# Optimization experiments

Measured on AMD Instinct MI355X. Metric: run time of the kernel, lower is better.

## Reference

```python
import jax, jax.numpy as jnp
import numpy as np

B, C, D, H, W = 2, 128, 16, 16, 16

def setup_inputs() -> dict:
    key = jax.random.key(0)
    ks = jax.random.split(key, 7)
    s = 0.02
    return {
        "x": jax.random.normal(ks[0], (B, C, D, H, W), jnp.float32),
        "Wq": jax.random.normal(ks[1], (C, C), jnp.float32) * s,
        "bq": jax.random.normal(ks[2], (C,), jnp.float32) * s,
        "Wk": jax.random.normal(ks[3], (C, C), jnp.float32) * s,
        "bk": jax.random.normal(ks[4], (C,), jnp.float32) * s,
        "Wv": jax.random.normal(ks[5], (C, C), jnp.float32) * s,
        "bv": jax.random.normal(ks[6], (C,), jnp.float32) * s,
    }

def reference(x, Wq, bq, Wk, bk, Wv, bv):
    b, c, d, h, w = x.shape
    n = d * h * w
    xf = x.reshape(b, c, n)  # [B, C, N]
    # 1x1x1 Conv3d == per-voxel linear over channels
    q = jnp.einsum('oc,bcn->bon', Wq, xf) + bq[None, :, None]
    k = jnp.einsum('oc,bcn->bon', Wk, xf) + bk[None, :, None]
    v = jnp.einsum('oc,bcn->bon', Wv, xf) + bv[None, :, None]
    # energy[b,n,m] = sum_c q[b,c,n] * k[b,c,m]  (no scale, as in source)
    energy = jnp.einsum('bcn,bcm->bnm', q, k)
    attention = jax.nn.softmax(energy, axis=-1)
    # out[b,c,n] = sum_m v[b,c,m] * attention[b,n,m]
    out = jnp.einsum('bcm,bnm->bcn', v, attention)
    return out.reshape(b, c, d, h, w)
```

## Files before the change

### kernel.cpp

```cpp
#include <hip/hip_runtime.h>


typedef __bf16 bf16x8 __attribute__((ext_vector_type(8)));
typedef __bf16 bf16x4v __attribute__((ext_vector_type(4)));
typedef float  f32x4  __attribute__((ext_vector_type(4)));

#define LDP 136
#define LDO 33

constexpr int CB = 128;
constexpr int NB = 4096;
constexpr int BB = 2;

__device__ __forceinline__ bf16x8 ldfrag(const __bf16* lds, int row, int koff, int ld) {
  return *(const bf16x8*)(lds + row * ld + koff);
}

__device__ __forceinline__ unsigned cvt_pk_bf16(float lo, float hi) {
  unsigned w;
  asm("v_cvt_pk_bf16_f32 %0, %1, %2" : "=v"(w) : "v"(lo), "v"(hi));
  return w;
}

__global__ __launch_bounds__(256) void qkv_proj_kernel(
    const float* __restrict__ x,
    const float* __restrict__ Wq, const float* __restrict__ bq,
    const float* __restrict__ Wk, const float* __restrict__ bk,
    const float* __restrict__ Wv, const float* __restrict__ bv,
    __bf16* __restrict__ Qt, __bf16* __restrict__ Kt, __bf16* __restrict__ Vo)
{
  extern __shared__ __align__(16) char smem_raw[];
  __bf16* xT = (__bf16*)smem_raw;
  __bf16* Wl = xT + 64 * LDP;

  const int b  = blockIdx.y;
  const int n0 = blockIdx.x * 64;
  const int m  = blockIdx.z;
  const int t  = threadIdx.x;
  const int lane = t & 63, w = t >> 6;
  const int l15 = lane & 15, quad = lane >> 4;

  const float* W = (m == 0) ? Wq : (m == 1) ? Wk : Wv;
  const float* bias_p = (m == 0) ? bq : (m == 1) ? bk : bv;
  const float qscale = (m == 0) ? 1.4426950408889634f : 1.0f;

  for (int v = t; v < 2048; v += 256) {
    int c = v >> 4, i4 = v & 15;
    float4 d = *(const float4*)(x + (b * CB + c) * NB + n0 + i4 * 4);
    xT[(i4 * 4 + 0) * LDP + c] = (__bf16)d.x;
    xT[(i4 * 4 + 1) * LDP + c] = (__bf16)d.y;
    xT[(i4 * 4 + 2) * LDP + c] = (__bf16)d.z;
    xT[(i4 * 4 + 3) * LDP + c] = (__bf16)d.w;
  }
  for (int v = t; v < 4096; v += 256) {
    int o = v >> 5, c4 = v & 31;
    float4 d = *(const float4*)(W + o * 128 + c4 * 4);
    bf16x4v u = {(__bf16)d.x, (__bf16)d.y, (__bf16)d.z, (__bf16)d.w};
    *(bf16x4v*)(Wl + o * LDP + c4 * 4) = u;
  }
  __syncthreads();

  if (m < 2) {
    f32x4 acc[8];
#pragma unroll
    for (int ct = 0; ct < 8; ct++) acc[ct] = (f32x4)0.0f;
#pragma unroll
    for (int ks = 0; ks < 4; ks++) {
      int koff = ks * 32 + quad * 8;
      bf16x8 a = ldfrag(xT, w * 16 + l15, koff, LDP);
#pragma unroll
      for (int ct = 0; ct < 8; ct++) {
        bf16x8 bb = ldfrag(Wl, ct * 16 + l15, koff, LDP);
        acc[ct] = __builtin_amdgcn_mfma_f32_16x16x32_bf16(a, bb, acc[ct], 0, 0, 0);
      }
    }
    __bf16* O = (m == 0) ? Qt : Kt;
#pragma unroll
    for (int ct = 0; ct < 8; ct++) {
      int o = ct * 16 + l15;
      float bias = bias_p[o];
#pragma unroll
      for (int r = 0; r < 4; r++) {
        int i = w * 16 + quad * 4 + r;
        O[(b * NB + n0 + i) * CB + o] = (__bf16)((acc[ct][r] + bias) * qscale);
      }
    }
  } else {
    f32x4 acc[2][4];
#pragma unroll
    for (int rr = 0; rr < 2; rr++)
#pragma unroll
      for (int ct = 0; ct < 4; ct++) acc[rr][ct] = (f32x4)0.0f;
#pragma unroll
    for (int ks = 0; ks < 4; ks++) {
      int koff = ks * 32 + quad * 8;
      bf16x8 a0 = ldfrag(Wl, (w * 2 + 0) * 16 + l15, koff, LDP);
      bf16x8 a1 = ldfrag(Wl, (w * 2 + 1) * 16 + l15, koff, LDP);
#pragma unroll
      for (int ct = 0; ct < 4; ct++) {
        bf16x8 bb = ldfrag(xT, ct * 16 + l15, koff, LDP);
        acc[0][ct] = __builtin_amdgcn_mfma_f32_16x16x32_bf16(a0, bb, acc[0][ct], 0, 0, 0);
        acc[1][ct] = __builtin_amdgcn_mfma_f32_16x16x32_bf16(a1, bb, acc[1][ct], 0, 0, 0);
      }
    }
#pragma unroll
    for (int rr = 0; rr < 2; rr++)
#pragma unroll
      for (int ct = 0; ct < 4; ct++)
#pragma unroll
        for (int r = 0; r < 4; r++) {
          int o = (w * 2 + rr) * 16 + quad * 4 + r;
          int i = ct * 16 + l15;
          Vo[(b * CB + o) * NB + n0 + i] = (__bf16)(acc[rr][ct][r] + bias_p[o]);
        }
  }
}

__global__ __launch_bounds__(256, 2) void attn_part_kernel(
    const __bf16* __restrict__ Qt,
    const __bf16* __restrict__ Kt,
    const __bf16* __restrict__ Vo,
    __bf16* __restrict__ Opart, float* __restrict__ Ll, int ksz)
{
  extern __shared__ __align__(16) char smem_raw[];

  const int b  = blockIdx.y;
  const int q0 = blockIdx.x * 128;
  const int s  = blockIdx.z;
  const int k_base = s * ksz;
  const int nit = ksz >> 6;
  const int t  = threadIdx.x;
  const int lane = t & 63, w = t >> 6;
  const int l15 = lane & 15, quad = lane >> 4;
  const int row0 = w * 32;
  const int xsw = (l15 & 7) << 4;

  bf16x8 qf[2][4];
#pragma unroll
  for (int qt = 0; qt < 2; qt++)
#pragma unroll
    for (int cb = 0; cb < 4; cb++)
      qf[qt][cb] = *(const bf16x8*)(Qt +
          (size_t)(b * NB + q0 + row0 + qt * 16 + l15) * CB + cb * 32 + quad * 8);

  bf16x8 kr[4], vr[4];
  auto load_tile = [&](int m0) {
#pragma unroll
    for (int u = 0; u < 4; u++) {
      int v = t + u * 256;
      int j = v >> 4, c8 = v & 15;
      kr[u] = *(const bf16x8*)(Kt + (size_t)(b * NB + m0 + j) * CB + c8 * 8);
    }
#pragma unroll
    for (int u = 0; u < 4; u++) {
      int v = t + u * 256;
      int c = v >> 3, j8 = v & 7;
      vr[u] = *(const bf16x8*)(Vo + (size_t)(b * CB + c) * NB + m0 + j8 * 8);
    }
  };
  auto write_tile = [&](int bf) {
    char* Kn = smem_raw + bf * 32768;
    char* Vn = Kn + 16384;
#pragma unroll
    for (int u = 0; u < 4; u++) {
      int v = t + u * 256;
      int j = v >> 4, c8 = v & 15;
      *(bf16x8*)(Kn + j * 256 + ((c8 * 16) ^ ((j & 7) << 4))) = kr[u];
    }
#pragma unroll
    for (int u = 0; u < 4; u++) {
      int v = t + u * 256;
      int c = v >> 3, j8 = v & 7;
      *(bf16x8*)(Vn + c * 128 + ((j8 * 16) ^ ((c & 7) << 4))) = vr[u];
    }
  };

  float lsum[2] = {0.0f, 0.0f};
  f32x4 o_acc[2][8];
#pragma unroll
  for (int qt = 0; qt < 2; qt++)
#pragma unroll
    for (int tt = 0; tt < 8; tt++) o_acc[qt][tt] = (f32x4)0.0f;

  load_tile(k_base);
  write_tile(0);
  __syncthreads();

  int cur = 0;
  for (int it = 0; it < nit; it++) {
    if (it + 1 < nit) load_tile(k_base + (it + 1) * 64);

    const char* Kc = smem_raw + cur * 32768;
    const char* Vc = Kc + 16384;

    f32x4 sacc[2][4];
#pragma unroll
    for (int qt = 0; qt < 2; qt++)
#pragma unroll
      for (int kt = 0; kt < 4; kt++) sacc[qt][kt] = (f32x4)0.0f;
#pragma unroll
    for (int cb = 0; cb < 4; cb++) {
      const int xo = (cb * 64 + quad * 16) ^ xsw;
#pragma unroll
      for (int kt = 0; kt < 4; kt++) {
        bf16x8 af = *(const bf16x8*)(Kc + (kt * 16 + l15) * 256 + xo);
        sacc[0][kt] = __builtin_amdgcn_mfma_f32_16x16x32_bf16(af, qf[0][cb], sacc[0][kt], 0, 0, 0);
        sacc[1][kt] = __builtin_amdgcn_mfma_f32_16x16x32_bf16(af, qf[1][cb], sacc[1][kt], 0, 0, 0);
      }
    }

    bf16x8 pa[2][2];
#pragma unroll
    for (int qt = 0; qt < 2; qt++) {
      unsigned d[4][2];
#pragma unroll
      for (int kt = 0; kt < 4; kt++) {
        float p0 = exp2f(sacc[qt][kt][0]);
        float p1 = exp2f(sacc[qt][kt][1]);
        float p2 = exp2f(sacc[qt][kt][2]);
        float p3 = exp2f(sacc[qt][kt][3]);
        lsum[qt] += (p0 + p1) + (p2 + p3);
        d[kt][0] = cvt_pk_bf16(p0, p1);
        d[kt][1] = cvt_pk_bf16(p2, p3);
      }
#pragma unroll
      for (int ks = 0; ks < 2; ks++) {
        unsigned a0 = d[2 * ks][0], a1 = d[2 * ks][1];
        unsigned b0 = d[2 * ks + 1][0], b1 = d[2 * ks + 1][1];
        asm("v_permlane32_swap_b32 %0, %1" : "+v"(a0), "+v"(b0));
        asm("v_permlane16_swap_b32 %0, %1" : "+v"(a0), "+v"(b0));
        asm("v_permlane32_swap_b32 %0, %1" : "+v"(a1), "+v"(b1));
        asm("v_permlane16_swap_b32 %0, %1" : "+v"(a1), "+v"(b1));
        union { unsigned u[4]; bf16x8 v; } pk;
        pk.u[0] = a0; pk.u[1] = a1; pk.u[2] = b0; pk.u[3] = b1;
        pa[qt][ks] = pk.v;
      }
    }

#pragma unroll
    for (int ks = 0; ks < 2; ks++) {
      const int xo = (ks * 64 + quad * 16) ^ xsw;
#pragma unroll
      for (int tt = 0; tt < 8; tt++) {
        bf16x8 bb = *(const bf16x8*)(Vc + (tt * 16 + l15) * 128 + xo);
        o_acc[0][tt] = __builtin_amdgcn_mfma_f32_16x16x32_bf16(pa[0][ks], bb, o_acc[0][tt], 0, 0, 0);
        o_acc[1][tt] = __builtin_amdgcn_mfma_f32_16x16x32_bf16(pa[1][ks], bb, o_acc[1][tt], 0, 0, 0);
      }
    }

    if (it + 1 < nit) {
      write_tile(cur ^ 1);
      __syncthreads();
      cur ^= 1;
    }
  }

#pragma unroll
  for (int qt = 0; qt < 2; qt++) {
    lsum[qt] += __shfl_xor(lsum[qt], 16);
    lsum[qt] += __shfl_xor(lsum[qt], 32);
  }

  const size_t obase = ((size_t)(s * BB + b) * NB + q0) * CB;
#pragma unroll
  for (int qt = 0; qt < 2; qt++)
#pragma unroll
    for (int tt = 0; tt < 8; tt++)
#pragma unroll
      for (int r = 0; r < 4; r++)
        Opart[obase + (size_t)(row0 + qt * 16 + quad * 4 + r) * CB + tt * 16 + l15] =
            (__bf16)o_acc[qt][tt][r];
  if (quad == 0) {
    const size_t lbase = (size_t)(s * BB + b) * NB + q0 + row0;
#pragma unroll
    for (int qt = 0; qt < 2; qt++)
      Ll[lbase + qt * 16 + l15] = lsum[qt];
  }
}

__global__ __launch_bounds__(256) void combine_kernel(
    const __bf16* __restrict__ Opart, const float* __restrict__ Ll,
    float* __restrict__ out, int nsplit)
{
  extern __shared__ __align__(16) char smem_raw[];
  float* Olf = (float*)smem_raw;

  const int b  = blockIdx.y;
  const int n0 = blockIdx.x * 64;
  const int c0 = blockIdx.z * 32;
  const int t  = threadIdx.x;
  const int i  = t >> 2;
  const int cc = (t & 3) * 8;

  float L = 0.0f;
  for (int s = 0; s < nsplit; s++)
    L += Ll[(size_t)(s * BB + b) * NB + n0 + i];

  float acc[8];
#pragma unroll
  for (int u = 0; u < 8; u++) acc[u] = 0.0f;
  for (int s = 0; s < nsplit; s++) {
    bf16x8 d = *(const bf16x8*)(Opart +
        ((size_t)(s * BB + b) * NB + n0 + i) * CB + c0 + cc);
#pragma unroll
    for (int u = 0; u < 8; u++) acc[u] += (float)d[u];
  }
  float invL = 1.0f / L;
#pragma unroll
  for (int u = 0; u < 8; u++) Olf[i * LDO + cc + u] = acc[u] * invL;
  __syncthreads();

  for (int v = t; v < 512; v += 256) {
    int c = v >> 4, i4 = v & 15;
    float4 d;
    d.x = Olf[(i4 * 4 + 0) * LDO + c];
    d.y = Olf[(i4 * 4 + 1) * LDO + c];
    d.z = Olf[(i4 * 4 + 2) * LDO + c];
    d.w = Olf[(i4 * 4 + 3) * LDO + c];
    *(float4*)(out + (size_t)(b * CB + c0 + c) * NB + n0 + i4 * 4) = d;
  }
}

extern "C" void kernel_launch(void* const* d_in, const int* in_sizes, int n_in,
                              void* d_out, int out_size, void* d_ws, size_t ws_size,
                              hipStream_t stream) {
  const float* x  = (const float*)d_in[0];
  const float* Wq = (const float*)d_in[1];
  const float* bq = (const float*)d_in[2];
  const float* Wk = (const float*)d_in[3];
  const float* bk = (const float*)d_in[4];
  const float* Wv = (const float*)d_in[5];
  const float* bv = (const float*)d_in[6];
  float* out = (float*)d_out;

  const size_t qkv_elems = (size_t)BB * NB * CB;
  __bf16* Qt = (__bf16*)d_ws;
  __bf16* Kt = Qt + qkv_elems;
  __bf16* Vo = Kt + qkv_elems;
  char* ws_tail = (char*)(Vo + qkv_elems);
  size_t tail_sz = ws_size - 3 * qkv_elems * sizeof(__bf16);

  const size_t per_split = (size_t)BB * NB * CB * 2 + (size_t)BB * NB * 4;
  int nsplit = 8;
  while (nsplit > 1 && (size_t)nsplit * per_split > tail_sz) nsplit >>= 1;

  __bf16* Opart = (__bf16*)ws_tail;
  float*  Ll = (float*)(Opart + (size_t)nsplit * BB * NB * CB);
  const int ksz = NB / nsplit;

  const int qkv_smem  = (64 * LDP + 128 * LDP) * 2;
  const int attn_smem = 65536;
  const int comb_smem = 64 * LDO * 4;

  qkv_proj_kernel<<<dim3(NB / 64, BB, 3), 256, qkv_smem, stream>>>(
      x, Wq, bq, Wk, bk, Wv, bv, Qt, Kt, Vo);
  attn_part_kernel<<<dim3(NB / 128, BB, nsplit), 256, attn_smem, stream>>>(
      Qt, Kt, Vo, Opart, Ll, ksz);
  combine_kernel<<<dim3(NB / 64, BB, 4), 256, comb_smem, stream>>>(
      Opart, Ll, out, nsplit);
}
```

Measured before the change: 112.4 us.

## Load V fragments directly from global memory instead of staging through LDS

In the attention kernel the V tile is no longer staged in shared memory. Each wave loads its MFMA B-operand fragments for V straight from global memory (and L2) inside the loop, and only K stays double-buffered in LDS. This halves shared memory per block, which may allow more resident blocks, and removes the V LDS writes and reads. The cost is that each of the four waves fetches the same V data from global memory, so V traffic rises and global load latency now sits inside the loop with no prefetch into LDS.

```diff
diff --git a/kernel.cpp b/kernel.cpp
--- a/kernel.cpp
+++ b/kernel.cpp
@@ -143,36 +143,25 @@
       qf[qt][cb] = *(const bf16x8*)(Qt +
           (size_t)(b * NB + q0 + row0 + qt * 16 + l15) * CB + cb * 32 + quad * 8);
 
-  bf16x8 kr[4], vr[4];
-  auto load_tile = [&](int m0) {
+  const __bf16* Vbase = Vo + (size_t)(b * CB + l15) * NB + quad * 8;
+
+  bf16x8 kr[4];
+  auto load_ktile = [&](int m0) {
 #pragma unroll
     for (int u = 0; u < 4; u++) {
       int v = t + u * 256;
       int j = v >> 4, c8 = v & 15;
       kr[u] = *(const bf16x8*)(Kt + (size_t)(b * NB + m0 + j) * CB + c8 * 8);
     }
-#pragma unroll
-    for (int u = 0; u < 4; u++) {
-      int v = t + u * 256;
-      int c = v >> 3, j8 = v & 7;
-      vr[u] = *(const bf16x8*)(Vo + (size_t)(b * CB + c) * NB + m0 + j8 * 8);
-    }
   };
-  auto write_tile = [&](int bf) {
-    char* Kn = smem_raw + bf * 32768;
-    char* Vn = Kn + 16384;
+  auto write_ktile = [&](int bf) {
+    char* Kn = smem_raw + bf * 16384;
 #pragma unroll
     for (int u = 0; u < 4; u++) {
       int v = t + u * 256;
       int j = v >> 4, c8 = v & 15;
       *(bf16x8*)(Kn + j * 256 + ((c8 * 16) ^ ((j & 7) << 4))) = kr[u];
     }
-#pragma unroll
-    for (int u = 0; u < 4; u++) {
-      int v = t + u * 256;
-      int c = v >> 3, j8 = v & 7;
-      *(bf16x8*)(Vn + c * 128 + ((j8 * 16) ^ ((c & 7) << 4))) = vr[u];
-    }
   };
 
   float lsum[2] = {0.0f, 0.0f};
@@ -182,16 +171,22 @@
 #pragma unroll
     for (int tt = 0; tt < 8; tt++) o_acc[qt][tt] = (f32x4)0.0f;
 
-  load_tile(k_base);
-  write_tile(0);
+  load_ktile(k_base);
+  write_ktile(0);
   __syncthreads();
 
   int cur = 0;
   for (int it = 0; it < nit; it++) {
-    if (it + 1 < nit) load_tile(k_base + (it + 1) * 64);
-
-    const char* Kc = smem_raw + cur * 32768;
-    const char* Vc = Kc + 16384;
+    const int m0 = k_base + it * 64;
+
+    if (it + 1 < nit) load_ktile(m0 + 64);
+
+    bf16x8 vb0[8];
+#pragma unroll
+    for (int tt = 0; tt < 8; tt++)
+      vb0[tt] = *(const bf16x8*)(Vbase + (size_t)(tt * 16) * NB + m0);
+
+    const char* Kc = smem_raw + cur * 16384;
 
     f32x4 sacc[2][4];
 #pragma unroll
@@ -237,19 +232,24 @@
       }
     }
 
-#pragma unroll
-    for (int ks = 0; ks < 2; ks++) {
-      const int xo = (ks * 64 + quad * 16) ^ xsw;
-#pragma unroll
-      for (int tt = 0; tt < 8; tt++) {
-        bf16x8 bb = *(const bf16x8*)(Vc + (tt * 16 + l15) * 128 + xo);
-        o_acc[0][tt] = __builtin_amdgcn_mfma_f32_16x16x32_bf16(pa[0][ks], bb, o_acc[0][tt], 0, 0, 0);
-        o_acc[1][tt] = __builtin_amdgcn_mfma_f32_16x16x32_bf16(pa[1][ks], bb, o_acc[1][tt], 0, 0, 0);
-      }
+    bf16x8 vb1[8];
+#pragma unroll
+    for (int tt = 0; tt < 8; tt++)
+      vb1[tt] = *(const bf16x8*)(Vbase + (size_t)(tt * 16) * NB + m0 + 32);
+
+#pragma unroll
+    for (int tt = 0; tt < 8; tt++) {
+      o_acc[0][tt] = __builtin_amdgcn_mfma_f32_16x16x32_bf16(pa[0][0], vb0[tt], o_acc[0][tt], 0, 0, 0);
+      o_acc[1][tt] = __builtin_amdgcn_mfma_f32_16x16x32_bf16(pa[1][0], vb0[tt], o_acc[1][tt], 0, 0, 0);
+    }
+#pragma unroll
+    for (int tt = 0; tt < 8; tt++) {
+      o_acc[0][tt] = __builtin_amdgcn_mfma_f32_16x16x32_bf16(pa[0][1], vb1[tt], o_acc[0][tt], 0, 0, 0);
+      o_acc[1][tt] = __builtin_amdgcn_mfma_f32_16x16x32_bf16(pa[1][1], vb1[tt], o_acc[1][tt], 0, 0, 0);
     }
 
     if (it + 1 < nit) {
-      write_tile(cur ^ 1);
+      write_ktile(cur ^ 1);
       __syncthreads();
       cur ^= 1;
     }
@@ -349,7 +349,7 @@
   const int ksz = NB / nsplit;
 
   const int qkv_smem  = (64 * LDP + 128 * LDP) * 2;
-  const int attn_smem = 65536;
+  const int attn_smem = 32768;
   const int comb_smem = 64 * LDO * 4;
 
   qkv_proj_kernel<<<dim3(NB / 64, BB, 3), 256, qkv_smem, stream>>>(
```

Result: slower. 128.8 us (+14.6%).

## Fuse Q/K/V projections into one block and coalesce stores via LDS bounce

Applied to the files above, without the earlier changes.

The three separate per-projection blocks become one block per 32-voxel tile that loads and converts x once, then loops over Wq, Wk and Wv. Accumulators are staged through an LDS bounce buffer so the global writes become 16-byte vectorized, coalesced stores. The store for one projection is overlapped with the weight load for the next. In exchange there are fewer and longer blocks, more LDS per block, and each block reloads all three weight matrices from global memory.

```diff
diff --git a/kernel.cpp b/kernel.cpp
--- a/kernel.cpp
+++ b/kernel.cpp
@@ -7,6 +7,8 @@
 
 #define LDP 136
 #define LDO 33
+#define QB_STRIDE 132
+#define VB_STRIDE 36
 
 constexpr int CB = 128;
 constexpr int NB = 4096;
@@ -22,7 +24,7 @@
   return w;
 }
 
-__global__ __launch_bounds__(256) void qkv_proj_kernel(
+__global__ __launch_bounds__(256) void qkv_fused_kernel(
     const float* __restrict__ x,
     const float* __restrict__ Wq, const float* __restrict__ bq,
     const float* __restrict__ Wk, const float* __restrict__ bk,
@@ -31,89 +33,128 @@
 {
   extern __shared__ __align__(16) char smem_raw[];
   __bf16* xT = (__bf16*)smem_raw;
-  __bf16* Wl = xT + 64 * LDP;
+  __bf16* Wl = xT + 32 * LDP;
+  float* bounce = (float*)(Wl + 128 * LDP);
 
   const int b  = blockIdx.y;
-  const int n0 = blockIdx.x * 64;
-  const int m  = blockIdx.z;
+  const int n0 = blockIdx.x * 32;
   const int t  = threadIdx.x;
   const int lane = t & 63, w = t >> 6;
   const int l15 = lane & 15, quad = lane >> 4;
-
-  const float* W = (m == 0) ? Wq : (m == 1) ? Wk : Wv;
-  const float* bias_p = (m == 0) ? bq : (m == 1) ? bk : bv;
-  const float qscale = (m == 0) ? 1.4426950408889634f : 1.0f;
-
-  for (int v = t; v < 2048; v += 256) {
-    int c = v >> 4, i4 = v & 15;
-    float4 d = *(const float4*)(x + (b * CB + c) * NB + n0 + i4 * 4);
+  const int nstrip = (w & 1) * 16;
+  const int obase  = (w >> 1) * 64;
+
+#pragma unroll
+  for (int u = 0; u < 4; u++) {
+    int v = t + u * 256;
+    int c = v >> 3, i4 = v & 7;
+    float4 d = *(const float4*)(x + (size_t)(b * CB + c) * NB + n0 + i4 * 4);
     xT[(i4 * 4 + 0) * LDP + c] = (__bf16)d.x;
     xT[(i4 * 4 + 1) * LDP + c] = (__bf16)d.y;
     xT[(i4 * 4 + 2) * LDP + c] = (__bf16)d.z;
     xT[(i4 * 4 + 3) * LDP + c] = (__bf16)d.w;
   }
-  for (int v = t; v < 4096; v += 256) {
-    int o = v >> 5, c4 = v & 31;
-    float4 d = *(const float4*)(W + o * 128 + c4 * 4);
-    bf16x4v u = {(__bf16)d.x, (__bf16)d.y, (__bf16)d.z, (__bf16)d.w};
-    *(bf16x4v*)(Wl + o * LDP + c4 * 4) = u;
-  }
-  __syncthreads();
-
-  if (m < 2) {
-    f32x4 acc[8];
-#pragma unroll
-    for (int ct = 0; ct < 8; ct++) acc[ct] = (f32x4)0.0f;
-#pragma unroll
-    for (int ks = 0; ks < 4; ks++) {
-      int koff = ks * 32 + quad * 8;
-      bf16x8 a = ldfrag(xT, w * 16 + l15, koff, LDP);
-#pragma unroll
-      for (int ct = 0; ct < 8; ct++) {
-        bf16x8 bb = ldfrag(Wl, ct * 16 + l15, koff, LDP);
-        acc[ct] = __builtin_amdgcn_mfma_f32_16x16x32_bf16(a, bb, acc[ct], 0, 0, 0);
-      }
-    }
-    __bf16* O = (m == 0) ? Qt : Kt;
-#pragma unroll
-    for (int ct = 0; ct < 8; ct++) {
-      int o = ct * 16 + l15;
-      float bias = bias_p[o];
-#pragma unroll
-      for (int r = 0; r < 4; r++) {
-        int i = w * 16 + quad * 4 + r;
-        O[(b * NB + n0 + i) * CB + o] = (__bf16)((acc[ct][r] + bias) * qscale);
-      }
-    }
-  } else {
-    f32x4 acc[2][4];
-#pragma unroll
-    for (int rr = 0; rr < 2; rr++)
-#pragma unroll
-      for (int ct = 0; ct < 4; ct++) acc[rr][ct] = (f32x4)0.0f;
-#pragma unroll
-    for (int ks = 0; ks < 4; ks++) {
-      int koff = ks * 32 + quad * 8;
-      bf16x8 a0 = ldfrag(Wl, (w * 2 + 0) * 16 + l15, koff, LDP);
-      bf16x8 a1 = ldfrag(Wl, (w * 2 + 1) * 16 + l15, koff, LDP);
-#pragma unroll
-      for (int ct = 0; ct < 4; ct++) {
-        bf16x8 bb = ldfrag(xT, ct * 16 + l15, koff, LDP);
-        acc[0][ct] = __builtin_amdgcn_mfma_f32_16x16x32_bf16(a0, bb, acc[0][ct], 0, 0, 0);
-        acc[1][ct] = __builtin_amdgcn_mfma_f32_16x16x32_bf16(a1, bb, acc[1][ct], 0, 0, 0);
-      }
-    }
-#pragma unroll
-    for (int rr = 0; rr < 2; rr++)
+
+  auto store_m = [&](int mm) {
+    if (mm < 2) {
+      const float* bp = (mm == 0) ? bq : bk;
+      const float qs = (mm == 0) ? 1.4426950408889634f : 1.0f;
+      __bf16* O = (mm == 0) ? Qt : Kt;
+#pragma unroll
+      for (int u = 0; u < 2; u++) {
+        int v = t + u * 256;
+        int n = v >> 4, c8 = (v & 15) * 8;
+        f32x4 p0 = *(const f32x4*)(bounce + n * QB_STRIDE + c8);
+        f32x4 p1 = *(const f32x4*)(bounce + n * QB_STRIDE + c8 + 4);
+        float4 b0 = *(const float4*)(bp + c8);
+        float4 b1 = *(const float4*)(bp + c8 + 4);
+        bf16x8 o8;
+        o8[0] = (__bf16)((p0[0] + b0.x) * qs);
+        o8[1] = (__bf16)((p0[1] + b0.y) * qs);
+        o8[2] = (__bf16)((p0[2] + b0.z) * qs);
+        o8[3] = (__bf16)((p0[3] + b0.w) * qs);
+        o8[4] = (__bf16)((p1[0] + b1.x) * qs);
+        o8[5] = (__bf16)((p1[1] + b1.y) * qs);
+        o8[6] = (__bf16)((p1[2] + b1.z) * qs);
+        o8[7] = (__bf16)((p1[3] + b1.w) * qs);
+        *(bf16x8*)(O + (size_t)(b * NB + n0 + n) * CB + c8) = o8;
+      }
+    } else {
+#pragma unroll
+      for (int u = 0; u < 2; u++) {
+        int v = t + u * 256;
+        int o = v >> 2, n8 = (v & 3) * 8;
+        float bias = bv[o];
+        f32x4 p0 = *(const f32x4*)(bounce + o * VB_STRIDE + n8);
+        f32x4 p1 = *(const f32x4*)(bounce + o * VB_STRIDE + n8 + 4);
+        bf16x8 o8;
+        o8[0] = (__bf16)(p0[0] + bias);
+        o8[1] = (__bf16)(p0[1] + bias);
+        o8[2] = (__bf16)(p0[2] + bias);
+        o8[3] = (__bf16)(p0[3] + bias);
+        o8[4] = (__bf16)(p1[0] + bias);
+        o8[5] = (__bf16)(p1[1] + bias);
+        o8[6] = (__bf16)(p1[2] + bias);
+        o8[7] = (__bf16)(p1[3] + bias);
+        *(bf16x8*)(Vo + (size_t)(b * CB + o) * NB + n0 + n8) = o8;
+      }
+    }
+  };
+
+#pragma unroll
+  for (int m = 0; m < 3; m++) {
+    const float* W = (m == 0) ? Wq : (m == 1) ? Wk : Wv;
+#pragma unroll
+    for (int u = 0; u < 16; u++) {
+      int v = t + u * 256;
+      int o = v >> 5, c4 = v & 31;
+      float4 d = *(const float4*)(W + o * 128 + c4 * 4);
+      bf16x4v uu = {(__bf16)d.x, (__bf16)d.y, (__bf16)d.z, (__bf16)d.w};
+      *(bf16x4v*)(Wl + o * LDP + c4 * 4) = uu;
+    }
+    if (m > 0) store_m(m - 1);
+    __syncthreads();
+
+    if (m < 2) {
+      f32x4 acc[4] = {(f32x4)0.0f, (f32x4)0.0f, (f32x4)0.0f, (f32x4)0.0f};
+#pragma unroll
+      for (int ks = 0; ks < 4; ks++) {
+        int koff = ks * 32 + quad * 8;
+        bf16x8 a = ldfrag(xT, nstrip + l15, koff, LDP);
+#pragma unroll
+        for (int ct = 0; ct < 4; ct++) {
+          bf16x8 bb = ldfrag(Wl, obase + ct * 16 + l15, koff, LDP);
+          acc[ct] = __builtin_amdgcn_mfma_f32_16x16x32_bf16(a, bb, acc[ct], 0, 0, 0);
+        }
+      }
 #pragma unroll
       for (int ct = 0; ct < 4; ct++)
 #pragma unroll
-        for (int r = 0; r < 4; r++) {
-          int o = (w * 2 + rr) * 16 + quad * 4 + r;
-          int i = ct * 16 + l15;
-          Vo[(b * CB + o) * NB + n0 + i] = (__bf16)(acc[rr][ct][r] + bias_p[o]);
+        for (int r = 0; r < 4; r++)
+          bounce[(nstrip + quad * 4 + r) * QB_STRIDE + obase + ct * 16 + l15] =
+              acc[ct][r];
+    } else {
+      f32x4 acc[4] = {(f32x4)0.0f, (f32x4)0.0f, (f32x4)0.0f, (f32x4)0.0f};
+#pragma unroll
+      for (int ks = 0; ks < 4; ks++) {
+        int koff = ks * 32 + quad * 8;
+        bf16x8 bb = ldfrag(xT, nstrip + l15, koff, LDP);
+#pragma unroll
+        for (int rr = 0; rr < 4; rr++) {
+          bf16x8 a = ldfrag(Wl, obase + rr * 16 + l15, koff, LDP);
+          acc[rr] = __builtin_amdgcn_mfma_f32_16x16x32_bf16(a, bb, acc[rr], 0, 0, 0);
         }
-  }
+      }
+#pragma unroll
+      for (int rr = 0; rr < 4; rr++)
+#pragma unroll
+        for (int r = 0; r < 4; r++)
+          bounce[(obase + rr * 16 + quad * 4 + r) * VB_STRIDE + nstrip + l15] =
+              acc[rr][r];
+    }
+    __syncthreads();
+  }
+  store_m(2);
 }
 
 __global__ __launch_bounds__(256, 2) void attn_part_kernel(
@@ -348,11 +389,11 @@
   float*  Ll = (float*)(Opart + (size_t)nsplit * BB * NB * CB);
   const int ksz = NB / nsplit;
 
-  const int qkv_smem  = (64 * LDP + 128 * LDP) * 2;
+  const int qkv_smem  = 32 * LDP * 2 + 128 * LDP * 2 + 128 * VB_STRIDE * 4;
   const int attn_smem = 65536;
   const int comb_smem = 64 * LDO * 4;
 
-  qkv_proj_kernel<<<dim3(NB / 64, BB, 3), 256, qkv_smem, stream>>>(
+  qkv_fused_kernel<<<dim3(NB / 32, BB), 256, qkv_smem, stream>>>(
       x, Wq, bq, Wk, bk, Wv, bv, Qt, Kt, Vo);
   attn_part_kernel<<<dim3(NB / 128, BB, nsplit), 256, attn_smem, stream>>>(
       Qt, Kt, Vo, Opart, Ll, ksz);
```

New measurement: 109.6 us, median of 2. 1.03x faster.
